# Performance work log

Hardware: AMD Instinct MI355X
Metric: run time of the kernel (lower is better)

Reference implementation:

```python
import jax, jax.numpy as jnp
import numpy as np

N_NODES = 100000
N_EDGES = 1600000
D_IN = 128
HIDDEN = 64
N_CLASSES = 10
N_GRAPHS = 512


def setup_inputs() -> dict:
    key = jax.random.key(0)
    ks = jax.random.split(key, 9)
    x = jax.random.normal(ks[0], (N_NODES, D_IN), dtype=jnp.float32)
    edge_index = jax.random.randint(ks[1], (2, N_EDGES), 0, N_NODES, dtype=jnp.int32)
    batch = jnp.sort(jax.random.randint(ks[2], (N_NODES,), 0, N_GRAPHS, dtype=jnp.int32))
    # GCNConv: lin (no bias) + separate bias added after aggregation
    s1 = 1.0 / np.sqrt(D_IN)
    s2 = 1.0 / np.sqrt(HIDDEN)
    W1 = jax.random.uniform(ks[3], (D_IN, HIDDEN), jnp.float32, -s1, s1)
    b1 = jnp.zeros((HIDDEN,), jnp.float32)
    W2 = jax.random.uniform(ks[4], (HIDDEN, HIDDEN), jnp.float32, -s2, s2)
    b2 = jnp.zeros((HIDDEN,), jnp.float32)
    Wfc = jax.random.uniform(ks[5], (HIDDEN, N_CLASSES), jnp.float32, -s2, s2)
    bfc = jax.random.uniform(ks[6], (N_CLASSES,), jnp.float32, -s2, s2)
    return {"x": x, "edge_index": edge_index, "batch": batch,
            "W1": W1, "b1": b1, "W2": W2, "b2": b2, "Wfc": Wfc, "bfc": bfc}


def gcn_conv(x, src, dst, W, b, n_nodes):
    # symmetric normalization with added self-loops (PyG gcn_norm defaults)
    deg = jnp.zeros((n_nodes,), x.dtype).at[dst].add(1.0) + 1.0  # +1 self-loop
    dinv = jax.lax.rsqrt(deg)
    h = x @ W  # [N, out]
    coef = (dinv[src] * dinv[dst])[:, None]          # [E, 1]
    msg = h[src] * coef                               # [E, out]
    agg = jax.ops.segment_sum(msg, dst, num_segments=n_nodes)
    agg = agg + h * (dinv * dinv)[:, None]            # self-loop contribution
    return agg + b


def reference(x, edge_index, batch, W1, b1, W2, b2, Wfc, bfc):
    src, dst = edge_index[0], edge_index[1]
    n_nodes = x.shape[0]
    h = gcn_conv(x, src, dst, W1, b1, n_nodes)
    h = jax.nn.relu(h)
    # dropout skipped (inference, training=False)
    h = gcn_conv(h, src, dst, W2, b2, n_nodes)
    h = jax.nn.relu(h)
    # global mean pool over graphs
    sums = jax.ops.segment_sum(h, batch, num_segments=N_GRAPHS)
    cnts = jax.ops.segment_sum(jnp.ones((n_nodes,), h.dtype), batch, num_segments=N_GRAPHS)
    pooled = sums / jnp.maximum(cnts, 1.0)[:, None]   # [G, hidden]
    logits = pooled @ Wfc + bfc                        # [G, classes]
    return jax.nn.log_softmax(logits, axis=1)
```

## Files before the change

kernel.cpp:

```cpp
#include <hip/hip_runtime.h>
#include <cstdint>
#include <cstddef>

#define N_NODES   100000
#define N_EDGES   1600000
#define D_IN      128
#define HIDDEN    64
#define N_GRAPHS  512
#define N_CLASSES 10

#define NB   196
#define EB4  391
#define BCAP 12288
#define PSLOTS 8

typedef __attribute__((ext_vector_type(8))) short bf16x8;
typedef __attribute__((ext_vector_type(4))) float f32x4;
typedef __attribute__((ext_vector_type(2))) float f32x2;

__device__ inline float bf2f(unsigned short u) {
    return __uint_as_float(((unsigned int)u) << 16);
}
__device__ inline unsigned short f2bf(float f) {
    unsigned int x = __float_as_uint(f);
    return (unsigned short)((x + 0x7FFF + ((x >> 16) & 1)) >> 16);
}

__global__ __launch_bounds__(256)
void hist2_kernel(const int* __restrict__ dst, int* __restrict__ bucketTot) {
    __shared__ int cnt[NB];
    const int tid = threadIdx.x;
    for (int i = tid; i < NB; i += 256) cnt[i] = 0;
    __syncthreads();
    int base = blockIdx.x * 4096 + tid;
#pragma unroll
    for (int j = 0; j < 16; j++) {
        int t = base + j * 256;
        if (t < N_EDGES) atomicAdd(&cnt[dst[t] >> 9], 1);
    }
    __syncthreads();
    for (int b = tid; b < NB; b += 256) {
        int c = cnt[b];
        if (c) atomicAdd(&bucketTot[b], c);
    }
}

__global__ __launch_bounds__(256)
void scan196_kernel(const int* __restrict__ bucketTot, int* __restrict__ bucketBase,
                    int* __restrict__ bucketCur) {
    __shared__ int lds[256];
    int tid = threadIdx.x;
    int v = (tid < NB) ? bucketTot[tid] : 0;
    lds[tid] = v; __syncthreads();
    for (int off = 1; off < 256; off <<= 1) {
        int t = (tid >= off) ? lds[tid - off] : 0;
        __syncthreads();
        lds[tid] += t;
        __syncthreads();
    }
    int ex = lds[tid] - v;
    if (tid < NB) { bucketBase[tid] = ex; bucketCur[tid] = ex; }
    if (tid == 255) bucketBase[NB] = lds[255];
}

__global__ __launch_bounds__(256)
void scatter_kernel(const int* __restrict__ src, const int* __restrict__ dst,
                    int* __restrict__ bucketCur, unsigned int* __restrict__ edgeA) {
    __shared__ unsigned int epk[4096];
    __shared__ unsigned char ebk[4096];
    __shared__ int cnt[NB];
    __shared__ int off[NB];
    int tid = threadIdx.x, blk = blockIdx.x;
    for (int i = tid; i < NB; i += 256) cnt[i] = 0;
    __syncthreads();
    int base = blk * 4096;
#pragma unroll
    for (int j = 0; j < 16; j++) {
        int li = j * 256 + tid;
        int t = base + li;
        if (t < N_EDGES) {
            int d = dst[t];
            epk[li] = (((unsigned int)(d & 511)) << 17) | (unsigned int)src[t];
            ebk[li] = (unsigned char)(d >> 9);
            atomicAdd(&cnt[d >> 9], 1);
        }
    }
    __syncthreads();
    for (int b = tid; b < NB; b += 256) {
        int c = cnt[b];
        off[b] = c ? atomicAdd(&bucketCur[b], c) : 0;
    }
    __syncthreads();
    int nmax = min(4096, N_EDGES - base);
    for (int li = tid; li < nmax; li += 256) {
        int b = ebk[li];
        int r = atomicAdd(&off[b], 1);
        edgeA[r] = epk[li];
    }
}

__global__ __launch_bounds__(256)
void passB_kernel(const int* __restrict__ bucketBase, const unsigned int* __restrict__ edgeA,
                  int* __restrict__ noffs, float* __restrict__ dinv,
                  int* __restrict__ srcs2) {
    __shared__ int hist[512];
    __shared__ int off[512];
    __shared__ int ps[256];
    __shared__ unsigned int eds[BCAP];
    __shared__ int srcs_l[BCAP];

    int tid = threadIdx.x, b = blockIdx.x;
    int e0 = bucketBase[b];
    int e1 = bucketBase[b + 1];
    int n0 = b << 9;
    int nn = min(512, N_NODES - n0);
    int len = e1 - e0;

    hist[tid] = 0; hist[tid + 256] = 0;
    __syncthreads();
    if (len <= BCAP) {
        for (int i = tid; i < len; i += 256) {
            unsigned int e = edgeA[e0 + i];
            eds[i] = e;
            atomicAdd(&hist[e >> 17], 1);
        }
    } else {
        for (int i = tid; i < len; i += 256) atomicAdd(&hist[edgeA[e0 + i] >> 17], 1);
    }
    __syncthreads();

    for (int n = tid; n < nn; n += 256) dinv[n0 + n] = rsqrtf((float)hist[n] + 1.0f);

    int a0 = hist[2 * tid], a1 = hist[2 * tid + 1];
    ps[tid] = a0 + a1;
    __syncthreads();
    for (int d = 1; d < 256; d <<= 1) {
        int v = (tid >= d) ? ps[tid - d] : 0;
        __syncthreads();
        ps[tid] += v;
        __syncthreads();
    }
    int pre = ps[tid] - (a0 + a1);
    off[2 * tid] = pre;
    off[2 * tid + 1] = pre + a0;
    __syncthreads();

    for (int n = tid; n < nn; n += 256) noffs[n0 + n] = e0 + off[n];
    if (b == NB - 1 && tid == 0) noffs[N_NODES] = N_EDGES;
    __syncthreads();

    if (len <= BCAP) {
        for (int i = tid; i < len; i += 256) {
            unsigned int e = eds[i];
            int r = atomicAdd(&off[e >> 17], 1);
            srcs_l[r] = (int)(e & 0x1FFFFu);
        }
        __syncthreads();
        for (int i = tid; i < len; i += 256) srcs2[e0 + i] = srcs_l[i];
    } else {
        for (int i = tid; i < len; i += 256) {
            unsigned int e = edgeA[e0 + i];
            int r = atomicAdd(&off[e >> 17], 1);
            srcs2[e0 + r] = (int)(e & 0x1FFFFu);
        }
    }
}

__global__ __launch_bounds__(512)
void gemm1_kernel(const float* __restrict__ X, const float* __restrict__ W,
                  const float* __restrict__ dinv, unsigned short* __restrict__ H,
                  int n_rows) {
    constexpr int K  = D_IN;
    constexpr int KP = K + 8;
    __shared__ unsigned short Wt[64 * KP];

    const int tid  = threadIdx.x;
    const int row0 = blockIdx.x * 128;

    for (int i = tid; i < K * 64; i += 512) {
        int k = i >> 6;
        int n = i & 63;
        Wt[n * KP + k] = f2bf(W[i]);
    }

    const int wave = tid >> 6;
    const int lane = tid & 63;
    const int lrow = lane & 15;
    const int quad = lane >> 4;
    const int m = wave * 16 + lrow;
    const int row = row0 + m;
    const bool valid = row < n_rows;

    float4 xa[8];
    if (valid) {
        const float4* xr4 = (const float4*)(X + (size_t)row * K);
#pragma unroll
        for (int kt = 0; kt < 4; kt++) {
            int q = (kt * 32 + quad * 8) >> 2;
            xa[2 * kt]     = xr4[q];
            xa[2 * kt + 1] = xr4[q + 1];
        }
    } else {
#pragma unroll
        for (int j = 0; j < 8; j++) xa[j] = make_float4(0.f, 0.f, 0.f, 0.f);
    }
    __syncthreads();

    f32x4 acc0 = {0.f, 0.f, 0.f, 0.f};
    f32x4 acc1 = {0.f, 0.f, 0.f, 0.f};
    f32x4 acc2 = {0.f, 0.f, 0.f, 0.f};
    f32x4 acc3 = {0.f, 0.f, 0.f, 0.f};

#pragma unroll
    for (int kt = 0; kt < 4; kt++) {
        int k0 = kt * 32 + quad * 8;
        const float* f = (const float*)&xa[2 * kt];
        bf16x8 a;
#pragma unroll
        for (int j = 0; j < 8; j++) a[j] = (short)f2bf(f[j]);
        bf16x8 b0 = *(const bf16x8*)&Wt[(0 * 16 + lrow) * KP + k0];
        bf16x8 b1 = *(const bf16x8*)&Wt[(1 * 16 + lrow) * KP + k0];
        bf16x8 b2 = *(const bf16x8*)&Wt[(2 * 16 + lrow) * KP + k0];
        bf16x8 b3 = *(const bf16x8*)&Wt[(3 * 16 + lrow) * KP + k0];
        acc0 = __builtin_amdgcn_mfma_f32_16x16x32_bf16(a, b0, acc0, 0, 0, 0);
        acc1 = __builtin_amdgcn_mfma_f32_16x16x32_bf16(a, b1, acc1, 0, 0, 0);
        acc2 = __builtin_amdgcn_mfma_f32_16x16x32_bf16(a, b2, acc2, 0, 0, 0);
        acc3 = __builtin_amdgcn_mfma_f32_16x16x32_bf16(a, b3, acc3, 0, 0, 0);
    }

    f32x4 accs[4] = {acc0, acc1, acc2, acc3};
#pragma unroll
    for (int r = 0; r < 4; r++) {
        int orow = row0 + wave * 16 + quad * 4 + r;
        if (orow < n_rows) {
            float dv = dinv[orow];
#pragma unroll
            for (int c = 0; c < 4; c++)
                H[(size_t)orow * 64 + c * 16 + lrow] = f2bf(accs[c][r] * dv);
        }
    }
}

__device__ inline void upk_add(int4 u, float* acc) {
    unsigned int a = (unsigned int)u.x, b = (unsigned int)u.y;
    unsigned int d = (unsigned int)u.z, e = (unsigned int)u.w;
    acc[0] += __uint_as_float(a << 16);
    acc[1] += __uint_as_float(a & 0xFFFF0000u);
    acc[2] += __uint_as_float(b << 16);
    acc[3] += __uint_as_float(b & 0xFFFF0000u);
    acc[4] += __uint_as_float(d << 16);
    acc[5] += __uint_as_float(d & 0xFFFF0000u);
    acc[6] += __uint_as_float(e << 16);
    acc[7] += __uint_as_float(e & 0xFFFF0000u);
}

__device__ inline void upk8_add(int2 u, float* acc) {
    f32x2 p0 = __builtin_amdgcn_cvt_pk_f32_fp8(u.x, false);
    f32x2 p1 = __builtin_amdgcn_cvt_pk_f32_fp8(u.x, true);
    f32x2 p2 = __builtin_amdgcn_cvt_pk_f32_fp8(u.y, false);
    f32x2 p3 = __builtin_amdgcn_cvt_pk_f32_fp8(u.y, true);
    acc[0] += p0.x; acc[1] += p0.y;
    acc[2] += p1.x; acc[3] += p1.y;
    acc[4] += p2.x; acc[5] += p2.y;
    acc[6] += p3.x; acc[7] += p3.y;
}

__global__ __launch_bounds__(512)
void gather1_gemm2_kernel(const int* __restrict__ offs, const int* __restrict__ srcs,
                          const float* __restrict__ dinv, const unsigned short* __restrict__ h,
                          const float* __restrict__ b1v, const float* __restrict__ W2,
                          unsigned char* __restrict__ H8, int n_nodes) {
    constexpr int KP = 72;
    __shared__ unsigned short Hs[64 * KP];
    __shared__ unsigned short Wt[64 * KP];

    const int tid   = threadIdx.x;
    const int node0 = blockIdx.x * 64;

    for (int i = tid; i < 64 * 64; i += 512) {
        int k = i >> 6;
        int n = i & 63;
        Wt[n * KP + k] = f2bf(W2[i]);
    }

    const int g    = tid >> 3;
    const int node = node0 + g;
    const int cg   = (tid & 7) * 8;

    float acc[8];
#pragma unroll
    for (int j = 0; j < 8; j++) acc[j] = 0.f;
    float dn = 0.f;

    if (node < n_nodes) {
        dn = dinv[node];
        int4 us = *(const int4*)(h + (size_t)node * 64 + cg);
        upk_add(us, acc);

        int i = offs[node];
        const int i1 = offs[node + 1];
        int rem = i1 - i;
        if (rem > 0) {
            int s[16];
#pragma unroll
            for (int j = 0; j < 16; j++) s[j] = srcs[i + (j < rem ? j : rem - 1)];
            while (rem > 0) {
                int4 u16[16];
#pragma unroll
                for (int j = 0; j < 16; j++)
                    u16[j] = *(const int4*)(h + (size_t)s[j] * 64 + cg);
                const int cur  = rem < 16 ? rem : 16;
                const int ni   = i + cur;
                const int nrem = rem - cur;
                if (nrem > 0) {
#pragma unroll
                    for (int j = 0; j < 16; j++)
                        s[j] = srcs[ni + (j < nrem ? j : nrem - 1)];
                }
#pragma unroll
                for (int j = 0; j < 16; j++) { if (j < cur) upk_add(u16[j], acc); }
                i = ni; rem = nrem;
            }
        }
    }

    {
        float4 bv0 = *(const float4*)(b1v + cg);
        float4 bv1 = *(const float4*)(b1v + cg + 4);
        float r0 = fmaxf(dn * acc[0] + bv0.x, 0.f);
        float r1 = fmaxf(dn * acc[1] + bv0.y, 0.f);
        float r2 = fmaxf(dn * acc[2] + bv0.z, 0.f);
        float r3 = fmaxf(dn * acc[3] + bv0.w, 0.f);
        float r4 = fmaxf(dn * acc[4] + bv1.x, 0.f);
        float r5 = fmaxf(dn * acc[5] + bv1.y, 0.f);
        float r6 = fmaxf(dn * acc[6] + bv1.z, 0.f);
        float r7 = fmaxf(dn * acc[7] + bv1.w, 0.f);
        ushort4 p0 = make_ushort4(f2bf(r0), f2bf(r1), f2bf(r2), f2bf(r3));
        ushort4 p1 = make_ushort4(f2bf(r4), f2bf(r5), f2bf(r6), f2bf(r7));
        *(ushort4*)&Hs[g * KP + cg]     = p0;
        *(ushort4*)&Hs[g * KP + cg + 4] = p1;
    }
    __syncthreads();

    const int wave = tid >> 6;
    const int lane = tid & 63;
    const int lrow = lane & 15;
    const int quad = lane >> 4;
    const int rt = (wave & 3) * 16;
    const int ct = (wave >> 2) * 32;
    const int m = rt + lrow;

    f32x4 acc0 = {0.f, 0.f, 0.f, 0.f};
    f32x4 acc1 = {0.f, 0.f, 0.f, 0.f};
#pragma unroll
    for (int kt = 0; kt < 2; kt++) {
        int k0 = kt * 32 + quad * 8;
        bf16x8 a  = *(const bf16x8*)&Hs[m * KP + k0];
        bf16x8 w0 = *(const bf16x8*)&Wt[(ct + lrow) * KP + k0];
        bf16x8 w1 = *(const bf16x8*)&Wt[(ct + 16 + lrow) * KP + k0];
        acc0 = __builtin_amdgcn_mfma_f32_16x16x32_bf16(a, w0, acc0, 0, 0, 0);
        acc1 = __builtin_amdgcn_mfma_f32_16x16x32_bf16(a, w1, acc1, 0, 0, 0);
    }

    f32x4 accs[2] = {acc0, acc1};
#pragma unroll
    for (int r = 0; r < 4; r++) {
        int row = node0 + rt + quad * 4 + r;
        if (row < n_nodes) {
            float dv = dinv[row];
#pragma unroll
            for (int c = 0; c < 2; c++) {
                float v = accs[c][r] * dv;
                int p = __builtin_amdgcn_cvt_pk_fp8_f32(v, v, 0, false);
                H8[(size_t)row * 64 + ct + c * 16 + lrow] = (unsigned char)(p & 0xFF);
            }
        }
    }
}

__global__ __launch_bounds__(256)
void gather_fp8_pool_kernel(const int* __restrict__ offs, const int* __restrict__ srcs,
                            const float* __restrict__ dinv, const unsigned char* __restrict__ h8,
                            const float* __restrict__ b, const int* __restrict__ batch,
                            float* __restrict__ pooled, float* __restrict__ cnt,
                            int n_nodes) {
    __shared__ float pacc[PSLOTS][64];
    __shared__ float lcnt[PSLOTS];
    __shared__ int sg[2];

    int tid = threadIdx.x;
    int node0 = blockIdx.x * 32;
    int lastn = min(node0 + 31, n_nodes - 1);
    for (int i = tid; i < PSLOTS * 64; i += 256) ((float*)pacc)[i] = 0.f;
    if (tid < PSLOTS) lcnt[tid] = 0.f;
    if (tid == 0) { sg[0] = batch[min(node0, n_nodes - 1)]; sg[1] = batch[lastn]; }
    __syncthreads();
    int g0 = sg[0];
    bool single = (sg[0] == sg[1]);

    int node = node0 + (tid >> 3);
    int cg = (tid & 7) * 8;

    float r[8];
#pragma unroll
    for (int j = 0; j < 8; j++) r[j] = 0.f;

    if (node < n_nodes) {
        float dn = dinv[node];
        float acc[8];
#pragma unroll
        for (int j = 0; j < 8; j++) acc[j] = 0.f;
        {
            int2 u = *(const int2*)(h8 + (size_t)node * 64 + cg);
            upk8_add(u, acc);
        }

        int i = offs[node];
        const int i1 = offs[node + 1];
        int rem = i1 - i;
        if (rem > 0) {
            int s[16];
#pragma unroll
            for (int j = 0; j < 16; j++) s[j] = srcs[i + (j < rem ? j : rem - 1)];
            while (rem > 0) {
                int2 u16[16];
#pragma unroll
                for (int j = 0; j < 16; j++)
                    u16[j] = *(const int2*)(h8 + (size_t)s[j] * 64 + cg);
                const int cur  = rem < 16 ? rem : 16;
                const int ni   = i + cur;
                const int nrem = rem - cur;
                if (nrem > 0) {
#pragma unroll
                    for (int j = 0; j < 16; j++)
                        s[j] = srcs[ni + (j < nrem ? j : nrem - 1)];
                }
#pragma unroll
                for (int j = 0; j < 16; j++) { if (j < cur) upk8_add(u16[j], acc); }
                i = ni; rem = nrem;
            }
        }

        float4 b0 = *(const float4*)(b + cg);
        float4 b1 = *(const float4*)(b + cg + 4);
        r[0] = fmaxf(dn * acc[0] + b0.x, 0.f);
        r[1] = fmaxf(dn * acc[1] + b0.y, 0.f);
        r[2] = fmaxf(dn * acc[2] + b0.z, 0.f);
        r[3] = fmaxf(dn * acc[3] + b0.w, 0.f);
        r[4] = fmaxf(dn * acc[4] + b1.x, 0.f);
        r[5] = fmaxf(dn * acc[5] + b1.y, 0.f);
        r[6] = fmaxf(dn * acc[6] + b1.z, 0.f);
        r[7] = fmaxf(dn * acc[7] + b1.w, 0.f);
    }

    if (single) {
#pragma unroll
        for (int j = 0; j < 8; j++) {
            float v = r[j];
            v += __shfl_xor(v, 8);
            v += __shfl_xor(v, 16);
            v += __shfl_xor(v, 32);
            r[j] = v;
        }
        int wave = tid >> 6;
        int lane = tid & 63;
        if (lane < 8) {
#pragma unroll
            for (int j = 0; j < 8; j++) pacc[wave][lane * 8 + j] = r[j];
        }
        __syncthreads();
        if (tid < 64) {
            float s = pacc[0][tid] + pacc[1][tid] + pacc[2][tid] + pacc[3][tid];
            if (s != 0.f) unsafeAtomicAdd(&pooled[(size_t)g0 * 64 + tid], s);
        }
        if (tid == 0) {
            int valid = min(32, n_nodes - node0);
            unsafeAtomicAdd(&cnt[g0], (float)valid);
        }
    } else {
        if (node < n_nodes) {
            int g = batch[node];
            int slot = g - g0;
            if (slot < PSLOTS) {
#pragma unroll
                for (int j = 0; j < 8; j++) atomicAdd(&pacc[slot][cg + j], r[j]);
                if ((tid & 7) == 0) atomicAdd(&lcnt[slot], 1.f);
            } else {
#pragma unroll
                for (int j = 0; j < 8; j++) unsafeAtomicAdd(&pooled[(size_t)g * 64 + cg + j], r[j]);
                if ((tid & 7) == 0) unsafeAtomicAdd(&cnt[g], 1.f);
            }
        }
        __syncthreads();
        for (int i = tid; i < PSLOTS * 64; i += 256) {
            float v = ((float*)pacc)[i];
            if (v != 0.f) unsafeAtomicAdd(&pooled[(size_t)(g0 + (i >> 6)) * 64 + (i & 63)], v);
        }
        if (tid < PSLOTS && lcnt[tid] != 0.f) unsafeAtomicAdd(&cnt[g0 + tid], lcnt[tid]);
    }
}

__global__ __launch_bounds__(256)
void head_kernel(const float* __restrict__ pooled, const float* __restrict__ cnt,
                 const float* __restrict__ Wfc, const float* __restrict__ bfc,
                 float* __restrict__ out) {
    __shared__ float Ws[HIDDEN * N_CLASSES];
    __shared__ float bs[N_CLASSES];
    int tid = threadIdx.x;
    for (int i = tid; i < HIDDEN * N_CLASSES; i += 256) Ws[i] = Wfc[i];
    if (tid < N_CLASSES) bs[tid] = bfc[tid];
    __syncthreads();

    int g = blockIdx.x * 256 + tid;
    if (g >= N_GRAPHS) return;

    float inv = 1.f / fmaxf(cnt[g], 1.f);
    float p[HIDDEN];
#pragma unroll
    for (int k = 0; k < HIDDEN; k++) p[k] = pooled[(size_t)g * 64 + k] * inv;

    float lg[N_CLASSES];
    float m = -1e30f;
#pragma unroll
    for (int j = 0; j < N_CLASSES; j++) {
        float a = bs[j];
#pragma unroll
        for (int k = 0; k < HIDDEN; k++) a += p[k] * Ws[k * N_CLASSES + j];
        lg[j] = a;
        m = fmaxf(m, a);
    }
    float s = 0.f;
#pragma unroll
    for (int j = 0; j < N_CLASSES; j++) s += __expf(lg[j] - m);
    float lse = m + __logf(s);
#pragma unroll
    for (int j = 0; j < N_CLASSES; j++) out[(size_t)g * N_CLASSES + j] = lg[j] - lse;
}

extern "C" void kernel_launch(void* const* d_in, const int* in_sizes, int n_in,
                              void* d_out, int out_size, void* d_ws, size_t ws_size,
                              hipStream_t stream) {
    const float* x   = (const float*)d_in[0];
    const int*   ei  = (const int*)d_in[1];
    const int*   bat = (const int*)d_in[2];
    const float* W1  = (const float*)d_in[3];
    const float* b1  = (const float*)d_in[4];
    const float* W2  = (const float*)d_in[5];
    const float* b2  = (const float*)d_in[6];
    const float* Wfc = (const float*)d_in[7];
    const float* bfc = (const float*)d_in[8];
    float* out = (float*)d_out;

    const int* src = ei;
    const int* dst = ei + N_EDGES;

    char* ws = (char*)d_ws;

    const size_t OFF_H     = 0;
    const size_t OFF_SRCS2 = 12800000;
    const size_t OFF_NOFFS = 19200000;
    const size_t OFF_DINV  = 19600016;
    const size_t OFF_BUFB  = 25600000;
    const size_t OFF_EDGEA = 38400000;
    const size_t OFF_POOL  = 44800000;
    const size_t OFF_CNT   = 44931072;
    const size_t OFF_BTOT  = 44933120;
    const size_t OFF_BBASE = 44933904;
    const size_t OFF_BCUR  = 44934692;

    unsigned short* hbuf  = (unsigned short*)(ws + OFF_H);
    int*   srcs2  = (int*)  (ws + OFF_SRCS2);
    int*   noffs  = (int*)  (ws + OFF_NOFFS);
    float* dinv   = (float*)(ws + OFF_DINV);
    unsigned char* hbuf8 = (unsigned char*)(ws + OFF_BUFB);
    unsigned int* edgeA = (unsigned int*)(ws + OFF_EDGEA);
    float* pooled = (float*)(ws + OFF_POOL);
    float* cnt    = (float*)(ws + OFF_CNT);
    int* bucketTot  = (int*)(ws + OFF_BTOT);
    int* bucketBase = (int*)(ws + OFF_BBASE);
    int* bucketCur  = (int*)(ws + OFF_BCUR);

    const int GATHER_BLOCKS = (N_NODES * 8 + 255) / 256;
    const int GEMM2_BLOCKS = (N_NODES + 63) / 64;
    const int GEMM1_BLOCKS = (N_NODES + 127) / 128;

    hipMemsetAsync(pooled, 0, (size_t)(131072 + 2048 + 784), stream);

    hist2_kernel<<<EB4, 256, 0, stream>>>(dst, bucketTot);
    scan196_kernel<<<1, 256, 0, stream>>>(bucketTot, bucketBase, bucketCur);
    scatter_kernel<<<EB4, 256, 0, stream>>>(src, dst, bucketCur, edgeA);
    passB_kernel<<<NB, 256, 0, stream>>>(bucketBase, edgeA, noffs, dinv, srcs2);
    gemm1_kernel<<<GEMM1_BLOCKS, 512, 0, stream>>>(x, W1, dinv, hbuf, N_NODES);
    gather1_gemm2_kernel<<<GEMM2_BLOCKS, 512, 0, stream>>>(
        noffs, srcs2, dinv, hbuf, b1, W2, hbuf8, N_NODES);
    gather_fp8_pool_kernel<<<GATHER_BLOCKS, 256, 0, stream>>>(
        noffs, srcs2, dinv, hbuf8, b2, bat, pooled, cnt, N_NODES);

    head_kernel<<<(N_GRAPHS + 255) / 256, 256, 0, stream>>>(pooled, cnt, Wfc, bfc, out);
}
```

Baseline: 257.2 us.

## Widen fp8 gather loads, shrink gather batch, drop passB edge staging

```diff
diff --git a/kernel.cpp b/kernel.cpp
--- a/kernel.cpp
+++ b/kernel.cpp
@@ -106,7 +106,6 @@
     __shared__ int hist[512];
     __shared__ int off[512];
     __shared__ int ps[256];
-    __shared__ unsigned int eds[BCAP];
     __shared__ int srcs_l[BCAP];
 
     int tid = threadIdx.x, b = blockIdx.x;
@@ -118,15 +117,7 @@
 
     hist[tid] = 0; hist[tid + 256] = 0;
     __syncthreads();
-    if (len <= BCAP) {
-        for (int i = tid; i < len; i += 256) {
-            unsigned int e = edgeA[e0 + i];
-            eds[i] = e;
-            atomicAdd(&hist[e >> 17], 1);
-        }
-    } else {
-        for (int i = tid; i < len; i += 256) atomicAdd(&hist[edgeA[e0 + i] >> 17], 1);
-    }
+    for (int i = e0 + tid; i < e1; i += 256) atomicAdd(&hist[edgeA[i] >> 17], 1);
     __syncthreads();
 
     for (int n = tid; n < nn; n += 256) dinv[n0 + n] = rsqrtf((float)hist[n] + 1.0f);
@@ -150,16 +141,16 @@
     __syncthreads();
 
     if (len <= BCAP) {
-        for (int i = tid; i < len; i += 256) {
-            unsigned int e = eds[i];
+        for (int i = e0 + tid; i < e1; i += 256) {
+            unsigned int e = edgeA[i];
             int r = atomicAdd(&off[e >> 17], 1);
             srcs_l[r] = (int)(e & 0x1FFFFu);
         }
         __syncthreads();
         for (int i = tid; i < len; i += 256) srcs2[e0 + i] = srcs_l[i];
     } else {
-        for (int i = tid; i < len; i += 256) {
-            unsigned int e = edgeA[e0 + i];
+        for (int i = e0 + tid; i < e1; i += 256) {
+            unsigned int e = edgeA[i];
             int r = atomicAdd(&off[e >> 17], 1);
             srcs2[e0 + r] = (int)(e & 0x1FFFFu);
         }
@@ -254,15 +245,16 @@
     acc[7] += __uint_as_float(e & 0xFFFF0000u);
 }
 
-__device__ inline void upk8_add(int2 u, float* acc) {
-    f32x2 p0 = __builtin_amdgcn_cvt_pk_f32_fp8(u.x, false);
-    f32x2 p1 = __builtin_amdgcn_cvt_pk_f32_fp8(u.x, true);
-    f32x2 p2 = __builtin_amdgcn_cvt_pk_f32_fp8(u.y, false);
-    f32x2 p3 = __builtin_amdgcn_cvt_pk_f32_fp8(u.y, true);
-    acc[0] += p0.x; acc[1] += p0.y;
-    acc[2] += p1.x; acc[3] += p1.y;
-    acc[4] += p2.x; acc[5] += p2.y;
-    acc[6] += p3.x; acc[7] += p3.y;
+__device__ inline void upk16_add(int4 u, float* acc) {
+    f32x2 p;
+    p = __builtin_amdgcn_cvt_pk_f32_fp8(u.x, false); acc[0]  += p.x; acc[1]  += p.y;
+    p = __builtin_amdgcn_cvt_pk_f32_fp8(u.x, true);  acc[2]  += p.x; acc[3]  += p.y;
+    p = __builtin_amdgcn_cvt_pk_f32_fp8(u.y, false); acc[4]  += p.x; acc[5]  += p.y;
+    p = __builtin_amdgcn_cvt_pk_f32_fp8(u.y, true);  acc[6]  += p.x; acc[7]  += p.y;
+    p = __builtin_amdgcn_cvt_pk_f32_fp8(u.z, false); acc[8]  += p.x; acc[9]  += p.y;
+    p = __builtin_amdgcn_cvt_pk_f32_fp8(u.z, true);  acc[10] += p.x; acc[11] += p.y;
+    p = __builtin_amdgcn_cvt_pk_f32_fp8(u.w, false); acc[12] += p.x; acc[13] += p.y;
+    p = __builtin_amdgcn_cvt_pk_f32_fp8(u.w, true);  acc[14] += p.x; acc[15] += p.y;
 }
 
 __global__ __launch_bounds__(512)
@@ -301,24 +293,24 @@
         const int i1 = offs[node + 1];
         int rem = i1 - i;
         if (rem > 0) {
-            int s[16];
-#pragma unroll
-            for (int j = 0; j < 16; j++) s[j] = srcs[i + (j < rem ? j : rem - 1)];
+            int s[8];
+#pragma unroll
+            for (int j = 0; j < 8; j++) s[j] = srcs[i + (j < rem ? j : rem - 1)];
             while (rem > 0) {
-                int4 u16[16];
-#pragma unroll
-                for (int j = 0; j < 16; j++)
-                    u16[j] = *(const int4*)(h + (size_t)s[j] * 64 + cg);
-                const int cur  = rem < 16 ? rem : 16;
+                int4 u8[8];
+#pragma unroll
+                for (int j = 0; j < 8; j++)
+                    u8[j] = *(const int4*)(h + (size_t)s[j] * 64 + cg);
+                const int cur  = rem < 8 ? rem : 8;
                 const int ni   = i + cur;
                 const int nrem = rem - cur;
                 if (nrem > 0) {
 #pragma unroll
-                    for (int j = 0; j < 16; j++)
+                    for (int j = 0; j < 8; j++)
                         s[j] = srcs[ni + (j < nrem ? j : nrem - 1)];
                 }
 #pragma unroll
-                for (int j = 0; j < 16; j++) { if (j < cur) upk_add(u16[j], acc); }
+                for (int j = 0; j < 8; j++) { if (j < cur) upk_add(u8[j], acc); }
                 i = ni; rem = nrem;
             }
         }
@@ -389,8 +381,8 @@
     __shared__ int sg[2];
 
     int tid = threadIdx.x;
-    int node0 = blockIdx.x * 32;
-    int lastn = min(node0 + 31, n_nodes - 1);
+    int node0 = blockIdx.x * 64;
+    int lastn = min(node0 + 63, n_nodes - 1);
     for (int i = tid; i < PSLOTS * 64; i += 256) ((float*)pacc)[i] = 0.f;
     if (tid < PSLOTS) lcnt[tid] = 0.f;
     if (tid == 0) { sg[0] = batch[min(node0, n_nodes - 1)]; sg[1] = batch[lastn]; }
@@ -398,75 +390,72 @@
     int g0 = sg[0];
     bool single = (sg[0] == sg[1]);
 
-    int node = node0 + (tid >> 3);
-    int cg = (tid & 7) * 8;
-
-    float r[8];
-#pragma unroll
-    for (int j = 0; j < 8; j++) r[j] = 0.f;
-
-    if (node < n_nodes) {
+    const int node = node0 + (tid >> 2);
+    const int cg = (tid & 3) * 16;
+    const bool valid = node < n_nodes;
+
+    float acc[16];
+#pragma unroll
+    for (int j = 0; j < 16; j++) acc[j] = 0.f;
+
+    if (valid) {
         float dn = dinv[node];
-        float acc[8];
-#pragma unroll
-        for (int j = 0; j < 8; j++) acc[j] = 0.f;
         {
-            int2 u = *(const int2*)(h8 + (size_t)node * 64 + cg);
-            upk8_add(u, acc);
+            int4 u = *(const int4*)(h8 + (size_t)node * 64 + cg);
+            upk16_add(u, acc);
         }
 
         int i = offs[node];
         const int i1 = offs[node + 1];
         int rem = i1 - i;
         if (rem > 0) {
-            int s[16];
-#pragma unroll
-            for (int j = 0; j < 16; j++) s[j] = srcs[i + (j < rem ? j : rem - 1)];
+            int s[8];
+#pragma unroll
+            for (int j = 0; j < 8; j++) s[j] = srcs[i + (j < rem ? j : rem - 1)];
             while (rem > 0) {
-                int2 u16[16];
-#pragma unroll
-                for (int j = 0; j < 16; j++)
-                    u16[j] = *(const int2*)(h8 + (size_t)s[j] * 64 + cg);
-                const int cur  = rem < 16 ? rem : 16;
+                int4 u8[8];
+#pragma unroll
+                for (int j = 0; j < 8; j++)
+                    u8[j] = *(const int4*)(h8 + (size_t)s[j] * 64 + cg);
+                const int cur  = rem < 8 ? rem : 8;
                 const int ni   = i + cur;
                 const int nrem = rem - cur;
                 if (nrem > 0) {
 #pragma unroll
-                    for (int j = 0; j < 16; j++)
+                    for (int j = 0; j < 8; j++)
                         s[j] = srcs[ni + (j < nrem ? j : nrem - 1)];
                 }
 #pragma unroll
-                for (int j = 0; j < 16; j++) { if (j < cur) upk8_add(u16[j], acc); }
+                for (int j = 0; j < 8; j++) { if (j < cur) upk16_add(u8[j], acc); }
                 i = ni; rem = nrem;
             }
         }
 
-        float4 b0 = *(const float4*)(b + cg);
-        float4 b1 = *(const float4*)(b + cg + 4);
-        r[0] = fmaxf(dn * acc[0] + b0.x, 0.f);
-        r[1] = fmaxf(dn * acc[1] + b0.y, 0.f);
-        r[2] = fmaxf(dn * acc[2] + b0.z, 0.f);
-        r[3] = fmaxf(dn * acc[3] + b0.w, 0.f);
-        r[4] = fmaxf(dn * acc[4] + b1.x, 0.f);
-        r[5] = fmaxf(dn * acc[5] + b1.y, 0.f);
-        r[6] = fmaxf(dn * acc[6] + b1.z, 0.f);
-        r[7] = fmaxf(dn * acc[7] + b1.w, 0.f);
+#pragma unroll
+        for (int q = 0; q < 4; q++) {
+            float4 bv = *(const float4*)(b + cg + q * 4);
+            acc[q * 4 + 0] = fmaxf(dn * acc[q * 4 + 0] + bv.x, 0.f);
+            acc[q * 4 + 1] = fmaxf(dn * acc[q * 4 + 1] + bv.y, 0.f);
+            acc[q * 4 + 2] = fmaxf(dn * acc[q * 4 + 2] + bv.z, 0.f);
+            acc[q * 4 + 3] = fmaxf(dn * acc[q * 4 + 3] + bv.w, 0.f);
+        }
     }
 
     if (single) {
 #pragma unroll
-        for (int j = 0; j < 8; j++) {
-            float v = r[j];
+        for (int j = 0; j < 16; j++) {
+            float v = acc[j];
+            v += __shfl_xor(v, 4);
             v += __shfl_xor(v, 8);
             v += __shfl_xor(v, 16);
             v += __shfl_xor(v, 32);
-            r[j] = v;
+            acc[j] = v;
         }
         int wave = tid >> 6;
         int lane = tid & 63;
-        if (lane < 8) {
-#pragma unroll
-            for (int j = 0; j < 8; j++) pacc[wave][lane * 8 + j] = r[j];
+        if (lane < 4) {
+#pragma unroll
+            for (int j = 0; j < 16; j++) pacc[wave][lane * 16 + j] = acc[j];
         }
         __syncthreads();
         if (tid < 64) {
@@ -474,21 +463,21 @@
             if (s != 0.f) unsafeAtomicAdd(&pooled[(size_t)g0 * 64 + tid], s);
         }
         if (tid == 0) {
-            int valid = min(32, n_nodes - node0);
-            unsafeAtomicAdd(&cnt[g0], (float)valid);
+            int nv = min(64, n_nodes - node0);
+            unsafeAtomicAdd(&cnt[g0], (float)nv);
         }
     } else {
-        if (node < n_nodes) {
+        if (valid) {
             int g = batch[node];
             int slot = g - g0;
             if (slot < PSLOTS) {
 #pragma unroll
-                for (int j = 0; j < 8; j++) atomicAdd(&pacc[slot][cg + j], r[j]);
-                if ((tid & 7) == 0) atomicAdd(&lcnt[slot], 1.f);
+                for (int j = 0; j < 16; j++) atomicAdd(&pacc[slot][cg + j], acc[j]);
+                if ((tid & 3) == 0) atomicAdd(&lcnt[slot], 1.f);
             } else {
 #pragma unroll
-                for (int j = 0; j < 8; j++) unsafeAtomicAdd(&pooled[(size_t)g * 64 + cg + j], r[j]);
-                if ((tid & 7) == 0) unsafeAtomicAdd(&cnt[g], 1.f);
+                for (int j = 0; j < 16; j++) unsafeAtomicAdd(&pooled[(size_t)g * 64 + cg + j], acc[j]);
+                if ((tid & 3) == 0) unsafeAtomicAdd(&cnt[g], 1.f);
             }
         }
         __syncthreads();
@@ -580,7 +569,7 @@
     int* bucketBase = (int*)(ws + OFF_BBASE);
     int* bucketCur  = (int*)(ws + OFF_BCUR);
 
-    const int GATHER_BLOCKS = (N_NODES * 8 + 255) / 256;
+    const int GATHER2_BLOCKS = (N_NODES * 4 + 255) / 256;
     const int GEMM2_BLOCKS = (N_NODES + 63) / 64;
     const int GEMM1_BLOCKS = (N_NODES + 127) / 128;
 
@@ -593,7 +582,7 @@
     gemm1_kernel<<<GEMM1_BLOCKS, 512, 0, stream>>>(x, W1, dinv, hbuf, N_NODES);
     gather1_gemm2_kernel<<<GEMM2_BLOCKS, 512, 0, stream>>>(
         noffs, srcs2, dinv, hbuf, b1, W2, hbuf8, N_NODES);
-    gather_fp8_pool_kernel<<<GATHER_BLOCKS, 256, 0, stream>>>(
+    gather_fp8_pool_kernel<<<GATHER2_BLOCKS, 256, 0, stream>>>(
         noffs, srcs2, dinv, hbuf8, b2, bat, pooled, cnt, N_NODES);
 
     head_kernel<<<(N_GRAPHS + 255) / 256, 256, 0, stream>>>(pooled, cnt, Wfc, bfc, out);
```

Measured after the change: 247.5 us. 1.04x faster.
